# Kernel tuning notes

Measured on AMD Instinct MI355X. Metric: run time of the kernel, lower is better.

The kernel has to match this reference:

```python
import jax, jax.numpy as jnp
import numpy as np


def _cdist(p, t):
    # p: [N,3], t: [N,3] -> euclidean distance matrix [N,N] (torch.cdist p=2)
    d2 = (jnp.sum(p * p, -1)[:, None] + jnp.sum(t * t, -1)[None, :]
          - 2.0 * (p @ t.T))
    return jnp.sqrt(jnp.maximum(d2, 1e-12))


def _greedy_match_cost(cost):
    # cost: [N,N]. For each row i in order, pick the cheapest unused column.
    N = cost.shape[0]

    def step(used, row):
        masked = jnp.where(used, jnp.inf, row)
        j = jnp.argmin(masked)
        c = masked[j]
        return used.at[j].set(True), c

    _, per_point_cost = jax.lax.scan(step, jnp.zeros(N, dtype=bool), cost)
    return jnp.mean(per_point_cost)


def setup_inputs() -> dict:
    key = jax.random.key(0)
    k1, k2 = jax.random.split(key)
    B, N = 8, 2048
    pred = jax.random.normal(k1, (B, N, 3), dtype=jnp.float32)
    target = jax.random.normal(k2, (B, N, 3), dtype=jnp.float32)
    return {"pred": pred, "target": target}


def reference(pred, target):
    # cost matrices per batch: [B,N,N]
    cost = jax.vmap(_cdist)(pred, target)
    emd = jax.vmap(_greedy_match_cost)(cost)  # [B]
    return jnp.mean(emd)
```

## Files before the change

### kernel.cpp

```cpp
#include <hip/hip_runtime.h>

#define NPTS 2048
#define TOPK 32
#define RPB  8
#define MAINBLKS 30
#define TAILROWS (NPTS - MAINBLKS * 64)

typedef float v2f __attribute__((ext_vector_type(2)));
typedef unsigned int u32;
typedef u32 v2u __attribute__((ext_vector_type(2)));
typedef unsigned long long u64;

static __device__ __forceinline__ u32 umin32(u32 a, u32 b) { return b < a ? b : a; }
static __device__ __forceinline__ u64 umin64(u64 a, u64 b) { return b < a ? b : a; }

template <int CTRL>
static __device__ __forceinline__ u32 dpp_min(u32 m) {
  return umin32(m, (u32)__builtin_amdgcn_mov_dpp((int)m, CTRL, 0xF, 0xF, true));
}
static __device__ __forceinline__ u32 x16_min(u32 m) {
#if __has_builtin(__builtin_amdgcn_permlane16_swap)
  auto r = __builtin_amdgcn_permlane16_swap((int)m, (int)m, false, false);
  return umin32(m, umin32((u32)r[0], (u32)r[1]));
#else
  return umin32(m, (u32)__builtin_amdgcn_ds_swizzle((int)m, 0x401F));
#endif
}
static __device__ __forceinline__ u32 x32_min(u32 m) {
#if __has_builtin(__builtin_amdgcn_permlane32_swap)
  auto r = __builtin_amdgcn_permlane32_swap((int)m, (int)m, false, false);
  return umin32(m, umin32((u32)r[0], (u32)r[1]));
#else
  return umin32(m, (u32)__shfl_xor((int)m, 32, 64));
#endif
}
static __device__ __forceinline__ u32 sext_bit(u32 mask, int c) {
#if __has_builtin(__builtin_amdgcn_sbfe)
  return (u32)__builtin_amdgcn_sbfe((int)mask, c, 1);
#else
  return (u32)(((int)(mask << (31 - c))) >> 31);
#endif
}

template <int CTRL>
static __device__ __forceinline__ u64 dpp_min64(u64 k) {
  unsigned lo = (unsigned)k, hi = (unsigned)(k >> 32);
  unsigned olo = (unsigned)__builtin_amdgcn_mov_dpp((int)lo, CTRL, 0xF, 0xF, true);
  unsigned ohi = (unsigned)__builtin_amdgcn_mov_dpp((int)hi, CTRL, 0xF, 0xF, true);
  return umin64(k, ((u64)ohi << 32) | olo);
}
static __device__ __forceinline__ u64 x16_min64(u64 k) {
  unsigned lo = (unsigned)k, hi = (unsigned)(k >> 32);
#if __has_builtin(__builtin_amdgcn_permlane16_swap)
  auto rlo = __builtin_amdgcn_permlane16_swap(lo, lo, false, false);
  auto rhi = __builtin_amdgcn_permlane16_swap(hi, hi, false, false);
  u64 a = ((u64)rhi[0] << 32) | rlo[0];
  u64 b = ((u64)rhi[1] << 32) | rlo[1];
  return umin64(k, umin64(a, b));
#else
  unsigned olo = (unsigned)__builtin_amdgcn_ds_swizzle((int)lo, 0x401F);
  unsigned ohi = (unsigned)__builtin_amdgcn_ds_swizzle((int)hi, 0x401F);
  return umin64(k, ((u64)ohi << 32) | olo);
#endif
}
static __device__ __forceinline__ u64 x32_min64(u64 k) {
  unsigned lo = (unsigned)k, hi = (unsigned)(k >> 32);
#if __has_builtin(__builtin_amdgcn_permlane32_swap)
  auto rlo = __builtin_amdgcn_permlane32_swap(lo, lo, false, false);
  auto rhi = __builtin_amdgcn_permlane32_swap(hi, hi, false, false);
  u64 a = ((u64)rhi[0] << 32) | rlo[0];
  u64 b = ((u64)rhi[1] << 32) | rlo[1];
  return umin64(k, umin64(a, b));
#else
  unsigned olo = (unsigned)__shfl_xor((int)lo, 32, 64);
  unsigned ohi = (unsigned)__shfl_xor((int)hi, 32, 64);
  return umin64(k, ((u64)ohi << 32) | olo);
#endif
}
static __device__ __forceinline__ u64 wave_min_u64(u64 k) {
  k = dpp_min64<0xB1>(k);
  k = dpp_min64<0x4E>(k);
  k = dpp_min64<0x141>(k);
  k = dpp_min64<0x140>(k);
  k = x16_min64(k);
  k = x32_min64(k);
  return k;
}

#define FOR16(M) M(0) M(1) M(2) M(3) M(4) M(5) M(6) M(7) \
                 M(8) M(9) M(10) M(11) M(12) M(13) M(14) M(15)

#define LOADP(h) \
  v2f TX##h, TY##h, TZ##h, TQ##h; \
  { float x0 = tb[6*h+0], y0 = tb[6*h+1], z0 = tb[6*h+2]; \
    float x1 = tb[6*h+3], y1 = tb[6*h+4], z1 = tb[6*h+5]; \
    TX##h = (v2f){x0, x1}; TY##h = (v2f){y0, y1}; TZ##h = (v2f){z0, z1}; \
    TQ##h = (v2f){x0*x0 + y0*y0 + z0*z0, x1*x1 + y1*y1 + z1*z1}; }

#define DISTK(h) u64 KA##h, KB##h; { \
  v2f dot = __builtin_elementwise_fma(TX##h, Xv, \
              __builtin_elementwise_fma(TY##h, Yv, TZ##h * Zv)); \
  v2f dd  = __builtin_elementwise_fma(m2v, dot, TQ##h); \
  v2f d2  = Qv + dd; \
  float c0 = fmaxf(d2.x, 1e-12f), c1 = fmaxf(d2.y, 1e-12f); \
  KA##h = ((u64)(u32)__float_as_int(c0) << 32) | (u32)(base + 2*(h)); \
  KB##h = ((u64)(u32)__float_as_int(c1) << 32) | (u32)(base + 2*(h) + 1); }

#define G4(a, b, c, d) umin64(umin64(a, b), umin64(c, d))
#define ZG(c, KV, RL) case (c): KV = own ? ~0ULL : KV; goto RL;

__global__ __launch_bounds__(64, 2) void emd_topk_kernel(
    const float* __restrict__ pred, const float* __restrict__ target,
    u64* __restrict__ lists) {
  const int blk = blockIdx.x;
  const int b  = blk / (NPTS / RPB);
  const int r0 = (blk % (NPTS / RPB)) * RPB;
  const int lane = threadIdx.x;
  const float* p = pred + (size_t)b * NPTS * 3;
  const float* t = target + (size_t)b * NPTS * 3;

  const float* tb = t + (size_t)lane * 32 * 3;
  FOR16(LOADP)
  const int base = lane << 5;
  const v2f m2v = {-2.f, -2.f};

#pragma unroll 1
  for (int rr = 0; rr < RPB; ++rr) {
    const int i = r0 + rr;
    const float X = p[3 * i], Y = p[3 * i + 1], Z = p[3 * i + 2];
    const float Q = fmaf(X, X, fmaf(Y, Y, Z * Z));
    const v2f Xv = {X, X}, Yv = {Y, Y}, Zv = {Z, Z}, Qv = {Q, Q};
    FOR16(DISTK)

    u64 g0 = G4(KA0, KB0, KA1, KB1),   g1 = G4(KA2, KB2, KA3, KB3);
    u64 g2 = G4(KA4, KB4, KA5, KB5),   g3 = G4(KA6, KB6, KA7, KB7);
    u64 g4 = G4(KA8, KB8, KA9, KB9),   g5 = G4(KA10, KB10, KA11, KB11);
    u64 g6 = G4(KA12, KB12, KA13, KB13), g7 = G4(KA14, KB14, KA15, KB15);
    u64 h0 = umin64(g0, g1), h1 = umin64(g2, g3);
    u64 h2 = umin64(g4, g5), h3 = umin64(g6, g7);
    u64 q0 = umin64(h0, h1), q1 = umin64(h2, h3);
    u64 root = umin64(q0, q1);

    u64* out = lists + ((size_t)b * NPTS + i) * TOPK;
#pragma unroll 1
    for (int e = 0; e < TOPK; ++e) {
      u64 m = wave_min_u64(root);
      if (lane == 0) out[e] = m;
      if (e == TOPK - 1) break;
      const u32 col = (u32)m & (u32)(NPTS - 1);
      const bool own = (lane == (int)(col >> 5));
      const u32 k5 = col & 31u;
      switch (k5) {
        ZG(0,  KA0,  R0) ZG(1,  KB0,  R0) ZG(2,  KA1,  R0) ZG(3,  KB1,  R0)
        ZG(4,  KA2,  R1) ZG(5,  KB2,  R1) ZG(6,  KA3,  R1) ZG(7,  KB3,  R1)
        ZG(8,  KA4,  R2) ZG(9,  KB4,  R2) ZG(10, KA5,  R2) ZG(11, KB5,  R2)
        ZG(12, KA6,  R3) ZG(13, KB6,  R3) ZG(14, KA7,  R3) ZG(15, KB7,  R3)
        ZG(16, KA8,  R4) ZG(17, KB8,  R4) ZG(18, KA9,  R4) ZG(19, KB9,  R4)
        ZG(20, KA10, R5) ZG(21, KB10, R5) ZG(22, KA11, R5) ZG(23, KB11, R5)
        ZG(24, KA12, R6) ZG(25, KB12, R6) ZG(26, KA13, R6) ZG(27, KB13, R6)
        ZG(28, KA14, R7) ZG(29, KB14, R7) ZG(30, KA15, R7) ZG(31, KB15, R7)
        default: __builtin_unreachable();
      }
      R0: g0 = G4(KA0, KB0, KA1, KB1);     h0 = umin64(g0, g1); q0 = umin64(h0, h1); root = umin64(q0, q1); continue;
      R1: g1 = G4(KA2, KB2, KA3, KB3);     h0 = umin64(g0, g1); q0 = umin64(h0, h1); root = umin64(q0, q1); continue;
      R2: g2 = G4(KA4, KB4, KA5, KB5);     h1 = umin64(g2, g3); q0 = umin64(h0, h1); root = umin64(q0, q1); continue;
      R3: g3 = G4(KA6, KB6, KA7, KB7);     h1 = umin64(g2, g3); q0 = umin64(h0, h1); root = umin64(q0, q1); continue;
      R4: g4 = G4(KA8, KB8, KA9, KB9);     h2 = umin64(g4, g5); q1 = umin64(h2, h3); root = umin64(q0, q1); continue;
      R5: g5 = G4(KA10, KB10, KA11, KB11); h2 = umin64(g4, g5); q1 = umin64(h2, h3); root = umin64(q0, q1); continue;
      R6: g6 = G4(KA12, KB12, KA13, KB13); h3 = umin64(g6, g7); q1 = umin64(h2, h3); root = umin64(q0, q1); continue;
      R7: g7 = G4(KA14, KB14, KA15, KB15); h3 = umin64(g6, g7); q1 = umin64(h2, h3); root = umin64(q0, q1); continue;
    }
  }
}


#define LD16(M) M(0) M(1) M(2) M(3) M(4) M(5) M(6) M(7) \
                M(8) M(9) M(10) M(11) M(12) M(13) M(14) M(15)
#define DECLA(j) uint4 A##j;
#define LDA(j)   A##j = Lr[j];
#define WRCD(j)  { dst[(2*(j)) * 64 + lane]     = ((u64)A##j.y << 32) | A##j.x; \
                   dst[(2*(j) + 1) * 64 + lane] = ((u64)A##j.w << 32) | A##j.z; }

#define CASCADE() { \
    int guard_ = 0; \
    while (true) { \
      bool changed_ = false; \
      if (!committed && !exh) { \
        int g2_ = 0; \
        while (true) { \
          u32 c_ = vclaim[col]; \
          if (c_ >= (u32)lane) break; \
          alive &= ~(1u << rank); \
          if (alive == 0u) { exh = true; break; } \
          rank = (u32)__ffs(alive) - 1u; \
          cur = cl[rank * 64 + lane]; \
          col = (u32)cur & 2047u; \
          atomicMin(&claimCur[col], (u32)lane); \
          changed_ = true; \
          if (++g2_ > 33) break; \
        } \
      } \
      if (__ballot(changed_) == 0ULL) break; \
      if (++guard_ > 3000) break; \
    } }

__global__ __launch_bounds__(256, 1) void emd_seq_kernel(
    const float* __restrict__ pred, const float* __restrict__ target,
    const u64* __restrict__ lists, float* __restrict__ batch_sums) {
  const int b = blockIdx.x;
  const int tid = threadIdx.x;
  const int w = tid >> 6, lane = tid & 63;
  const float* t = target + (size_t)b * NPTS * 3;
  const float* p = pred + (size_t)b * NPTS * 3;

  __shared__ float4 tt[NPTS];
  __shared__ u64 cl64s[2][TOPK * 64];
  __shared__ u32 claimb[2][NPTS];
  __shared__ u32 fl[NPTS];
  __shared__ u32 sbitmap[64];
  __shared__ float4 ppredb[2][64];
  __shared__ float4 tpred[TAILROWS];

  for (int j = tid; j < NPTS; j += 256) {
    float x = t[3 * j], y = t[3 * j + 1], z = t[3 * j + 2];
    tt[((j & 31) << 6) | ((j >> 5) ^ (j & 31))] =
        make_float4(x, y, z, fmaf(x, x, fmaf(y, y, z * z)));
  }
  if (tid < 64) sbitmap[tid] = 0u;

  const u64* L = lists + (size_t)b * NPTS * TOPK;
  volatile u32* sbm = sbitmap;
  float psum = 0.f;

  const uint4* Lr;
  LD16(DECLA)

  if (w == 1) {
    Lr = (const uint4*)(L + (size_t)lane * TOPK);
    LD16(LDA)
    u64* dst = &cl64s[0][0];
    LD16(WRCD)
    Lr = (const uint4*)(L + (size_t)(64 + lane) * TOPK);
    LD16(LDA)
  } else if (w == 2) {
#pragma unroll
    for (int k = 0; k < 32; ++k) claimb[0][k * 64 + lane] = ~0u;
  } else if (w == 3) {
    { const float* pr = p + (size_t)lane * 3;
      float X = pr[0], Y = pr[1], Z = pr[2];
      ppredb[0][lane] = make_float4(X, Y, Z, fmaf(X, X, fmaf(Y, Y, Z * Z))); }
    { const float* pr = p + (size_t)(MAINBLKS * 64 + lane) * 3;
      float X = pr[0], Y = pr[1], Z = pr[2];
      tpred[lane] = make_float4(X, Y, Z, fmaf(X, X, fmaf(Y, Y, Z * Z))); }
    { const float* pr = p + (size_t)(MAINBLKS * 64 + 64 + lane) * 3;
      float X = pr[0], Y = pr[1], Z = pr[2];
      tpred[64 + lane] = make_float4(X, Y, Z, fmaf(X, X, fmaf(Y, Y, Z * Z))); }
  }

#pragma unroll 1
  for (int blk = 0; blk < MAINBLKS; ++blk) {
    __syncthreads();

    if (w == 1) {
      if (blk + 1 < MAINBLKS) {
        u64* dst = &cl64s[(blk + 1) & 1][0];
        LD16(WRCD)
        if (blk + 2 < MAINBLKS) {
          Lr = (const uint4*)(L + (size_t)((blk + 2) * 64 + lane) * TOPK);
          LD16(LDA)
        }
      }
    } else if (w == 2) {
      if (blk + 1 < MAINBLKS) {
#pragma unroll
        for (int k = 0; k < 32; ++k) claimb[(blk + 1) & 1][k * 64 + lane] = ~0u;
      }
    } else if (w == 3) {
      if (blk + 1 < MAINBLKS) {
        const float* pr = p + (size_t)((blk + 1) * 64 + lane) * 3;
        float X = pr[0], Y = pr[1], Z = pr[2];
        ppredb[(blk + 1) & 1][lane] =
            make_float4(X, Y, Z, fmaf(X, X, fmaf(Y, Y, Z * Z)));
      }
    } else {
      const u64* cl = &cl64s[blk & 1][0];
      u32* claimCur = &claimb[blk & 1][0];
      volatile u32* vclaim = claimCur;
      const float4* ppcur = &ppredb[blk & 1][0];

      u32 alive = 0u;
#pragma unroll
      for (int j = 0; j < 32; ++j) {
        u32 c = (u32)cl[j * 64 + lane] & 2047u;
        u32 wd = sbm[c >> 5];
        alive |= ((~(wd >> (c & 31u))) & 1u) << j;
      }

      bool committed = false;
      bool exh = (alive == 0u);
      u32 rank = 0, col = 0;
      u64 cur = 0;
      if (!exh) {
        rank = (u32)__ffs(alive) - 1u;
        cur = cl[rank * 64 + lane];
        col = (u32)cur & 2047u;
        atomicMin(&claimCur[col], (u32)lane);
      }
      CASCADE()

      bool flBuilt = false;
      u32 F = 0;
      int oguard = 0;
#pragma unroll 1
      while (true) {
        u64 exbl = __ballot(exh && !committed);
        if (exbl == 0ULL) break;
        int rstar = __ffsll(exbl) - 1;

        if (!committed && !exh && lane < rstar) {
          atomicOr(&sbitmap[col >> 5], 1u << (col & 31u));
          psum += sqrtf(__uint_as_float((u32)(cur >> 32)));
          committed = true;
        }

        if (!flBuilt) {
          u32 fw = ~sbm[lane];
          u32 cnt = __popc(fw);
          u32 pfx = cnt;
#pragma unroll
          for (int d = 1; d < 64; d <<= 1) {
            u32 o = (u32)__shfl_up((int)pfx, d, 64);
            if (lane >= d) pfx += o;
          }
          F = (u32)__shfl((int)pfx, 63, 64);
          pfx -= cnt;
          while (fw) {
            int bpos = __ffs(fw) - 1;
            fw &= fw - 1u;
            fl[pfx++] = ((u32)lane << 5) + (u32)bpos;
          }
          flBuilt = true;
        }

        u32 cst;
        {
          float4 P4 = ppcur[rstar];
          float X = P4.x, Y = P4.y, Z = P4.z, Q = P4.w;
          u64 mb = ~0ULL;
          for (u32 k = (u32)lane; k < F; k += 64) {
            u32 c = fl[k];
            u32 used = (sbm[c >> 5] >> (c & 31u)) & 1u;
            float4 c4 = tt[((c & 31u) << 6) | ((c >> 5) ^ (c & 31u))];
            float dot = fmaf(c4.x, X, fmaf(c4.y, Y, c4.z * Z));
            float d2 = Q + fmaf(-2.f, dot, c4.w);
            d2 = fmaxf(d2, 1e-12f);
            u64 kk = ((u64)(u32)__float_as_int(d2) << 32) | c;
            if (used) kk = ~0ULL;
            mb = umin64(mb, kk);
          }
          mb = wave_min_u64(mb);
          cst = (u32)mb & 2047u;
          if (lane == rstar) {
            psum += sqrtf(__uint_as_float((u32)(mb >> 32)));
            committed = true;
          }
        }
        u32 prev = vclaim[cst];
        if (lane == rstar) {
          atomicOr(&sbitmap[cst >> 5], 1u << (cst & 31u));
          atomicMin(&claimCur[cst], (u32)rstar);
        }
        if (prev != ~0u) {
          CASCADE()
        }
        if (++oguard > 80) break;
      }

      if (!committed) {
        atomicOr(&sbitmap[col >> 5], 1u << (col & 31u));
        psum += sqrtf(__uint_as_float((u32)(cur >> 32)));
      }
    }
  }

  __syncthreads();

  if (w == 0) {
    u32 fw = ~sbm[lane];
    u32 cnt = __popc(fw);
    u32 pfx = cnt;
#pragma unroll
    for (int d = 1; d < 64; d <<= 1) {
      u32 o = (u32)__shfl_up((int)pfx, d, 64);
      if (lane >= d) pfx += o;
    }
    u32 F = (u32)__shfl((int)pfx, 63, 64);
    pfx -= cnt;
    while (fw) {
      int bpos = __ffs(fw) - 1;
      fw &= fw - 1u;
      fl[pfx++] = ((u32)lane << 5) + (u32)bpos;
    }

    bool l0 = (u32)lane < F, l1 = (u32)(64 + lane) < F;
    u32 c0 = l0 ? fl[lane] : 0u;
    u32 c1 = l1 ? fl[64 + lane] : 0u;
    float4 t0 = tt[((c0 & 31u) << 6) | ((c0 >> 5) ^ (c0 & 31u))];
    float4 t1 = tt[((c1 & 31u) << 6) | ((c1 >> 5) ^ (c1 & 31u))];

#pragma unroll 1
    for (int r = 0; r < TAILROWS; ++r) {
      float4 P = tpred[r];
      float X = P.x, Y = P.y, Z = P.z, Q = P.w;
      float dot0 = fmaf(t0.x, X, fmaf(t0.y, Y, t0.z * Z));
      float d20 = fmaxf(Q + fmaf(-2.f, dot0, t0.w), 1e-12f);
      float dot1 = fmaf(t1.x, X, fmaf(t1.y, Y, t1.z * Z));
      float d21 = fmaxf(Q + fmaf(-2.f, dot1, t1.w), 1e-12f);
      u64 k0 = l0 ? (((u64)(u32)__float_as_int(d20) << 32) | c0) : ~0ULL;
      u64 k1 = l1 ? (((u64)(u32)__float_as_int(d21) << 32) | c1) : ~0ULL;
      u64 k = wave_min_u64(umin64(k0, k1));
      u32 wc = (u32)k & 2047u;
      l0 = l0 && (c0 != wc);
      l1 = l1 && (c1 != wc);
      if (lane == 0) psum += sqrtf(__uint_as_float((u32)(k >> 32)));
    }

    float v = psum;
    v += __shfl_xor(v, 1, 64);
    v += __shfl_xor(v, 2, 64);
    v += __shfl_xor(v, 4, 64);
    v += __shfl_xor(v, 8, 64);
    v += __shfl_xor(v, 16, 64);
    v += __shfl_xor(v, 32, 64);
    if (lane == 0) batch_sums[b] = v;
  }
}

#define DECLRU(h) v2u RU##h;
#define DIST(h) { \
  v2f dot = __builtin_elementwise_fma(TX##h, Xv, \
              __builtin_elementwise_fma(TY##h, Yv, TZ##h * Zv)); \
  v2f dd  = __builtin_elementwise_fma(m2v, dot, TQ##h); \
  v2f d2  = Qv + dd; \
  RU##h = (v2u){(u32)__float_as_int(d2.x), (u32)__float_as_int(d2.y)}; }
#define TOUR(h, c) { \
  u32 u0 = RU##h.x | sext_bit(usedmask, 2*h); \
  u32 u1 = RU##h.y | sext_bit(usedmask, 2*h + 1); \
  u32 pu = umin32(u0, u1); \
  u32 pk = (u1 < u0) ? (u32)(2*h + 1) : (u32)(2*h); \
  if (pu < bc##c) { bc##c = pu; kc##c = pk; } }

__global__ __launch_bounds__(64, 1) void emd_greedy_kernel(
    const float* __restrict__ pred, const float* __restrict__ target,
    float* __restrict__ batch_sums) {
  const int b = blockIdx.x, lane = threadIdx.x;
  const float* p = pred + (size_t)b * NPTS * 3;
  const float* t = target + (size_t)b * NPTS * 3;
  __shared__ float4 pp[NPTS + 2];
  for (int i = lane; i < NPTS; i += 64) {
    float x = p[3 * i], y = p[3 * i + 1], z = p[3 * i + 2];
    pp[i] = make_float4(x, y, z, x * x + y * y + z * z);
  }
  if (lane < 2) pp[NPTS + lane] = make_float4(0.f, 0.f, 0.f, 0.f);
  const float* tb = t + (size_t)lane * 32 * 3;
  FOR16(LOADP)
  FOR16(DECLRU)
  u32 usedmask = 0;
  float sum = 0.f;
  __syncthreads();
  const v2f m2v = {-2.f, -2.f};
  v2f Xv, Yv, Zv, Qv;
  {
    float4 A = pp[0];
    Xv = (v2f){A.x, A.x}; Yv = (v2f){A.y, A.y};
    Zv = (v2f){A.z, A.z}; Qv = (v2f){A.w, A.w};
    FOR16(DIST)
  }
  for (int i = 0; i < NPTS; ++i) {
    float4 An = pp[i + 1];
    u32 bc0 = ~0u, bc1 = ~0u, bc2 = ~0u, bc3 = ~0u;
    u32 kc0 = 0, kc1 = 0, kc2 = 0, kc3 = 0;
    TOUR(0, 0)  TOUR(1, 0)  TOUR(2, 0)  TOUR(3, 0)
    TOUR(4, 1)  TOUR(5, 1)  TOUR(6, 1)  TOUR(7, 1)
    TOUR(8, 2)  TOUR(9, 2)  TOUR(10, 2) TOUR(11, 2)
    TOUR(12, 3) TOUR(13, 3) TOUR(14, 3) TOUR(15, 3)
    bool s01 = bc1 < bc0; u32 v01 = s01 ? bc1 : bc0; u32 i01 = s01 ? kc1 : kc0;
    bool s23 = bc3 < bc2; u32 v23 = s23 ? bc3 : bc2; u32 i23 = s23 ? kc3 : kc2;
    bool sf  = v23 < v01; u32 bu  = sf ? v23 : v01; u32 bk  = sf ? i23 : i01;
    Xv = (v2f){An.x, An.x}; Yv = (v2f){An.y, An.y};
    Zv = (v2f){An.z, An.z}; Qv = (v2f){An.w, An.w};
    FOR16(DIST)
    u32 m = bu;
    m = dpp_min<0xB1>(m); m = dpp_min<0x4E>(m);
    m = dpp_min<0x141>(m); m = dpp_min<0x140>(m);
    m = x16_min(m); m = x32_min(m);
    u64 mk = __ballot(bu == m);
    int first = __ffsll(mk) - 1;
    usedmask |= (lane == first) ? (1u << bk) : 0u;
    sum += sqrtf(fmaxf(__uint_as_float(m), 1e-12f));
  }
  if (lane == 0) batch_sums[b] = sum;
}

__global__ void emd_finalize_kernel(const float* __restrict__ batch_sums,
                                    float* __restrict__ out, int B) {
  float acc = 0.f;
  for (int b = 0; b < B; ++b) acc += batch_sums[b] / (float)NPTS;
  out[0] = acc / (float)B;
}

extern "C" void kernel_launch(void* const* d_in, const int* in_sizes, int n_in,
                              void* d_out, int out_size, void* d_ws, size_t ws_size,
                              hipStream_t stream) {
  const float* pred   = (const float*)d_in[0];
  const float* target = (const float*)d_in[1];
  float* out = (float*)d_out;
  const int B = in_sizes[0] / (NPTS * 3);

  const size_t need = 256 + (size_t)B * NPTS * TOPK * sizeof(u64);
  if (ws_size >= need) {
    float* bs = (float*)d_ws;
    u64* lists = (u64*)((char*)d_ws + 256);
    emd_topk_kernel<<<B * (NPTS / RPB), 64, 0, stream>>>(pred, target, lists);
    emd_seq_kernel<<<B, 256, 0, stream>>>(pred, target, lists, bs);
    emd_finalize_kernel<<<1, 1, 0, stream>>>(bs, out, B);
  } else {
    float* bs = (float*)d_ws;
    emd_greedy_kernel<<<B, 64, 0, stream>>>(pred, target, bs);
    emd_finalize_kernel<<<1, 1, 0, stream>>>(bs, out, B);
  }
}
```

Baseline: 397.6 us.

## Split sequential matching kernel in two launches and rework claim cascade

```diff
diff --git a/kernel.cpp b/kernel.cpp
--- a/kernel.cpp
+++ b/kernel.cpp
@@ -4,6 +4,7 @@
 #define TOPK 32
 #define RPB  8
 #define MAINBLKS 30
+#define SPLITB 20
 #define TAILROWS (NPTS - MAINBLKS * 64)
 
 typedef float v2f __attribute__((ext_vector_type(2)));
@@ -181,32 +182,43 @@
 #define WRCD(j)  { dst[(2*(j)) * 64 + lane]     = ((u64)A##j.y << 32) | A##j.x; \
                    dst[(2*(j) + 1) * 64 + lane] = ((u64)A##j.w << 32) | A##j.z; }
 
+#define ADVANCE() { \
+    alive &= ~(1u << rank); \
+    if (alive == 0u) { exh = true; } \
+    else { \
+      rank = (u32)__ffs(alive) - 1u; \
+      cur = cl[rank * 64 + lane]; \
+      col = (u32)cur & 2047u; \
+    } }
+
 #define CASCADE() { \
     int guard_ = 0; \
     while (true) { \
       bool changed_ = false; \
       if (!committed && !exh) { \
+        if (holding && vclaim[col] < (u32)lane) { \
+          holding = false; \
+          ADVANCE() \
+          changed_ = true; \
+        } \
         int g2_ = 0; \
-        while (true) { \
-          u32 c_ = vclaim[col]; \
-          if (c_ >= (u32)lane) break; \
-          alive &= ~(1u << rank); \
-          if (alive == 0u) { exh = true; break; } \
-          rank = (u32)__ffs(alive) - 1u; \
-          cur = cl[rank * 64 + lane]; \
-          col = (u32)cur & 2047u; \
-          atomicMin(&claimCur[col], (u32)lane); \
+        while (!holding && !exh) { \
+          u32 old_ = atomicMin(&claimCur[col], (u32)lane); \
+          if (old_ >= (u32)lane) { holding = true; break; } \
+          ADVANCE() \
           changed_ = true; \
-          if (++g2_ > 33) break; \
+          if (++g2_ > 40) break; \
         } \
       } \
       if (__ballot(changed_) == 0ULL) break; \
       if (++guard_ > 3000) break; \
     } }
 
-__global__ __launch_bounds__(256, 1) void emd_seq_kernel(
+template <int BLK0, int BLK1, bool DOTAIL>
+__global__ __launch_bounds__(256, 1) void emd_seq_part(
     const float* __restrict__ pred, const float* __restrict__ target,
-    const u64* __restrict__ lists, float* __restrict__ batch_sums) {
+    const u64* __restrict__ lists, u32* __restrict__ bmws,
+    float* __restrict__ psumws, float* __restrict__ batch_sums) {
   const int b = blockIdx.x;
   const int tid = threadIdx.x;
   const int w = tid >> 6, lane = tid & 63;
@@ -226,7 +238,7 @@
     tt[((j & 31) << 6) | ((j >> 5) ^ (j & 31))] =
         make_float4(x, y, z, fmaf(x, x, fmaf(y, y, z * z)));
   }
-  if (tid < 64) sbitmap[tid] = 0u;
+  if (tid < 64) sbitmap[tid] = (BLK0 == 0) ? 0u : bmws[b * 64 + tid];
 
   const u64* L = lists + (size_t)b * NPTS * TOPK;
   volatile u32* sbm = sbitmap;
@@ -236,47 +248,51 @@
   LD16(DECLA)
 
   if (w == 1) {
-    Lr = (const uint4*)(L + (size_t)lane * TOPK);
+    Lr = (const uint4*)(L + (size_t)(BLK0 * 64 + lane) * TOPK);
     LD16(LDA)
-    u64* dst = &cl64s[0][0];
+    u64* dst = &cl64s[BLK0 & 1][0];
     LD16(WRCD)
-    Lr = (const uint4*)(L + (size_t)(64 + lane) * TOPK);
-    LD16(LDA)
+    if (BLK0 + 1 < BLK1) {
+      Lr = (const uint4*)(L + (size_t)((BLK0 + 1) * 64 + lane) * TOPK);
+      LD16(LDA)
+    }
   } else if (w == 2) {
 #pragma unroll
-    for (int k = 0; k < 32; ++k) claimb[0][k * 64 + lane] = ~0u;
+    for (int k = 0; k < 32; ++k) claimb[BLK0 & 1][k * 64 + lane] = ~0u;
   } else if (w == 3) {
-    { const float* pr = p + (size_t)lane * 3;
+    { const float* pr = p + (size_t)(BLK0 * 64 + lane) * 3;
       float X = pr[0], Y = pr[1], Z = pr[2];
-      ppredb[0][lane] = make_float4(X, Y, Z, fmaf(X, X, fmaf(Y, Y, Z * Z))); }
-    { const float* pr = p + (size_t)(MAINBLKS * 64 + lane) * 3;
-      float X = pr[0], Y = pr[1], Z = pr[2];
-      tpred[lane] = make_float4(X, Y, Z, fmaf(X, X, fmaf(Y, Y, Z * Z))); }
-    { const float* pr = p + (size_t)(MAINBLKS * 64 + 64 + lane) * 3;
-      float X = pr[0], Y = pr[1], Z = pr[2];
-      tpred[64 + lane] = make_float4(X, Y, Z, fmaf(X, X, fmaf(Y, Y, Z * Z))); }
+      ppredb[BLK0 & 1][lane] = make_float4(X, Y, Z, fmaf(X, X, fmaf(Y, Y, Z * Z))); }
+    if (DOTAIL) {
+      { const float* pr = p + (size_t)(MAINBLKS * 64 + lane) * 3;
+        float X = pr[0], Y = pr[1], Z = pr[2];
+        tpred[lane] = make_float4(X, Y, Z, fmaf(X, X, fmaf(Y, Y, Z * Z))); }
+      { const float* pr = p + (size_t)(MAINBLKS * 64 + 64 + lane) * 3;
+        float X = pr[0], Y = pr[1], Z = pr[2];
+        tpred[64 + lane] = make_float4(X, Y, Z, fmaf(X, X, fmaf(Y, Y, Z * Z))); }
+    }
   }
 
 #pragma unroll 1
-  for (int blk = 0; blk < MAINBLKS; ++blk) {
+  for (int blk = BLK0; blk < BLK1; ++blk) {
     __syncthreads();
 
     if (w == 1) {
-      if (blk + 1 < MAINBLKS) {
+      if (blk + 1 < BLK1) {
         u64* dst = &cl64s[(blk + 1) & 1][0];
         LD16(WRCD)
-        if (blk + 2 < MAINBLKS) {
+        if (blk + 2 < BLK1) {
           Lr = (const uint4*)(L + (size_t)((blk + 2) * 64 + lane) * TOPK);
           LD16(LDA)
         }
       }
     } else if (w == 2) {
-      if (blk + 1 < MAINBLKS) {
+      if (blk + 1 < BLK1) {
 #pragma unroll
         for (int k = 0; k < 32; ++k) claimb[(blk + 1) & 1][k * 64 + lane] = ~0u;
       }
     } else if (w == 3) {
-      if (blk + 1 < MAINBLKS) {
+      if (blk + 1 < BLK1) {
         const float* pr = p + (size_t)((blk + 1) * 64 + lane) * 3;
         float X = pr[0], Y = pr[1], Z = pr[2];
         ppredb[(blk + 1) & 1][lane] =
@@ -297,6 +313,7 @@
       }
 
       bool committed = false;
+      bool holding = false;
       bool exh = (alive == 0u);
       u32 rank = 0, col = 0;
       u64 cur = 0;
@@ -304,7 +321,6 @@
         rank = (u32)__ffs(alive) - 1u;
         cur = cl[rank * 64 + lane];
         col = (u32)cur & 2047u;
-        atomicMin(&claimCur[col], (u32)lane);
       }
       CASCADE()
 
@@ -386,53 +402,65 @@
   __syncthreads();
 
   if (w == 0) {
-    u32 fw = ~sbm[lane];
-    u32 cnt = __popc(fw);
-    u32 pfx = cnt;
+    if (DOTAIL) {
+      u32 fw = ~sbm[lane];
+      u32 cnt = __popc(fw);
+      u32 pfx = cnt;
 #pragma unroll
-    for (int d = 1; d < 64; d <<= 1) {
-      u32 o = (u32)__shfl_up((int)pfx, d, 64);
-      if (lane >= d) pfx += o;
+      for (int d = 1; d < 64; d <<= 1) {
+        u32 o = (u32)__shfl_up((int)pfx, d, 64);
+        if (lane >= d) pfx += o;
+      }
+      u32 F = (u32)__shfl((int)pfx, 63, 64);
+      pfx -= cnt;
+      while (fw) {
+        int bpos = __ffs(fw) - 1;
+        fw &= fw - 1u;
+        fl[pfx++] = ((u32)lane << 5) + (u32)bpos;
+      }
+
+      bool l0 = (u32)lane < F, l1 = (u32)(64 + lane) < F;
+      u32 c0 = l0 ? fl[lane] : 0u;
+      u32 c1 = l1 ? fl[64 + lane] : 0u;
+      float4 t0 = tt[((c0 & 31u) << 6) | ((c0 >> 5) ^ (c0 & 31u))];
+      float4 t1 = tt[((c1 & 31u) << 6) | ((c1 >> 5) ^ (c1 & 31u))];
+
+#pragma unroll 1
+      for (int r = 0; r < TAILROWS; ++r) {
+        float4 P = tpred[r];
+        float X = P.x, Y = P.y, Z = P.z, Q = P.w;
+        float dot0 = fmaf(t0.x, X, fmaf(t0.y, Y, t0.z * Z));
+        float d20 = fmaxf(Q + fmaf(-2.f, dot0, t0.w), 1e-12f);
+        float dot1 = fmaf(t1.x, X, fmaf(t1.y, Y, t1.z * Z));
+        float d21 = fmaxf(Q + fmaf(-2.f, dot1, t1.w), 1e-12f);
+        u64 k0 = l0 ? (((u64)(u32)__float_as_int(d20) << 32) | c0) : ~0ULL;
+        u64 k1 = l1 ? (((u64)(u32)__float_as_int(d21) << 32) | c1) : ~0ULL;
+        u64 k = wave_min_u64(umin64(k0, k1));
+        u32 wc = (u32)k & 2047u;
+        l0 = l0 && (c0 != wc);
+        l1 = l1 && (c1 != wc);
+        if (lane == 0) psum += sqrtf(__uint_as_float((u32)(k >> 32)));
+      }
+
+      float v = psum;
+      v += __shfl_xor(v, 1, 64);
+      v += __shfl_xor(v, 2, 64);
+      v += __shfl_xor(v, 4, 64);
+      v += __shfl_xor(v, 8, 64);
+      v += __shfl_xor(v, 16, 64);
+      v += __shfl_xor(v, 32, 64);
+      if (lane == 0) batch_sums[b] = v + psumws[b];
+    } else {
+      bmws[b * 64 + lane] = sbitmap[lane];
+      float v = psum;
+      v += __shfl_xor(v, 1, 64);
+      v += __shfl_xor(v, 2, 64);
+      v += __shfl_xor(v, 4, 64);
+      v += __shfl_xor(v, 8, 64);
+      v += __shfl_xor(v, 16, 64);
+      v += __shfl_xor(v, 32, 64);
+      if (lane == 0) psumws[b] = v;
     }
-    u32 F = (u32)__shfl((int)pfx, 63, 64);
-    pfx -= cnt;
-    while (fw) {
-      int bpos = __ffs(fw) - 1;
-      fw &= fw - 1u;
-      fl[pfx++] = ((u32)lane << 5) + (u32)bpos;
-    }
-
-    bool l0 = (u32)lane < F, l1 = (u32)(64 + lane) < F;
-    u32 c0 = l0 ? fl[lane] : 0u;
-    u32 c1 = l1 ? fl[64 + lane] : 0u;
-    float4 t0 = tt[((c0 & 31u) << 6) | ((c0 >> 5) ^ (c0 & 31u))];
-    float4 t1 = tt[((c1 & 31u) << 6) | ((c1 >> 5) ^ (c1 & 31u))];
-
-#pragma unroll 1
-    for (int r = 0; r < TAILROWS; ++r) {
-      float4 P = tpred[r];
-      float X = P.x, Y = P.y, Z = P.z, Q = P.w;
-      float dot0 = fmaf(t0.x, X, fmaf(t0.y, Y, t0.z * Z));
-      float d20 = fmaxf(Q + fmaf(-2.f, dot0, t0.w), 1e-12f);
-      float dot1 = fmaf(t1.x, X, fmaf(t1.y, Y, t1.z * Z));
-      float d21 = fmaxf(Q + fmaf(-2.f, dot1, t1.w), 1e-12f);
-      u64 k0 = l0 ? (((u64)(u32)__float_as_int(d20) << 32) | c0) : ~0ULL;
-      u64 k1 = l1 ? (((u64)(u32)__float_as_int(d21) << 32) | c1) : ~0ULL;
-      u64 k = wave_min_u64(umin64(k0, k1));
-      u32 wc = (u32)k & 2047u;
-      l0 = l0 && (c0 != wc);
-      l1 = l1 && (c1 != wc);
-      if (lane == 0) psum += sqrtf(__uint_as_float((u32)(k >> 32)));
-    }
-
-    float v = psum;
-    v += __shfl_xor(v, 1, 64);
-    v += __shfl_xor(v, 2, 64);
-    v += __shfl_xor(v, 4, 64);
-    v += __shfl_xor(v, 8, 64);
-    v += __shfl_xor(v, 16, 64);
-    v += __shfl_xor(v, 32, 64);
-    if (lane == 0) batch_sums[b] = v;
   }
 }
 
@@ -517,12 +545,18 @@
   float* out = (float*)d_out;
   const int B = in_sizes[0] / (NPTS * 3);
 
-  const size_t need = 256 + (size_t)B * NPTS * TOPK * sizeof(u64);
+  const size_t listsBytes = (size_t)B * NPTS * TOPK * sizeof(u64);
+  const size_t need = 256 + listsBytes + (size_t)B * (64 * 4 + 16);
   if (ws_size >= need) {
     float* bs = (float*)d_ws;
     u64* lists = (u64*)((char*)d_ws + 256);
+    u32* bmws = (u32*)((char*)d_ws + 256 + listsBytes);
+    float* psumws = (float*)((char*)d_ws + 256 + listsBytes + (size_t)B * 64 * 4);
     emd_topk_kernel<<<B * (NPTS / RPB), 64, 0, stream>>>(pred, target, lists);
-    emd_seq_kernel<<<B, 256, 0, stream>>>(pred, target, lists, bs);
+    emd_seq_part<0, SPLITB, false><<<B, 256, 0, stream>>>(
+        pred, target, lists, bmws, psumws, bs);
+    emd_seq_part<SPLITB, MAINBLKS, true><<<B, 256, 0, stream>>>(
+        pred, target, lists, bmws, psumws, bs);
     emd_finalize_kernel<<<1, 1, 0, stream>>>(bs, out, B);
   } else {
     float* bs = (float*)d_ws;
```

Measured after the change: 412.7 us. 3.8% more time.
